# Optimization experiments

Measured on AMD Instinct MI355X. Metric: run time of the kernel, lower is better.

The kernel has to match this reference:

```python
import jax, jax.numpy as jnp
import numpy as np
from jax import lax

BN_EPS = 1e-5

def conv1x1(x, w, b):
    # x: [B,C,T,H,W], w: [O,C], b: [O] -> [B,O,T,H,W]
    return jnp.einsum('oc,bcthw->bothw', w, x) + b[None, :, None, None, None]

def maxpool_1x2x2(x):
    # MaxPool3d(kernel=(1,2,2)), stride = kernel
    return lax.reduce_window(x, -jnp.inf, lax.max,
                             window_dimensions=(1, 1, 1, 2, 2),
                             window_strides=(1, 1, 1, 2, 2),
                             padding='VALID')

def setup_inputs() -> dict:
    key = jax.random.key(0)
    ks = jax.random.split(key, 16)
    B, C, T, H, W = 4, 256, 8, 32, 32
    Ci = 128
    s_in = 1.0 / np.sqrt(C)
    s_mid = 1.0 / np.sqrt(Ci)
    return {
        'x': jax.random.normal(ks[0], (B, C, T, H, W), jnp.float32),
        'w_theta': jax.random.normal(ks[1], (Ci, C), jnp.float32) * s_in,
        'b_theta': jax.random.normal(ks[2], (Ci,), jnp.float32) * 0.01,
        'w_phi': jax.random.normal(ks[3], (Ci, C), jnp.float32) * s_in,
        'b_phi': jax.random.normal(ks[4], (Ci,), jnp.float32) * 0.01,
        'w_g': jax.random.normal(ks[5], (Ci, C), jnp.float32) * s_in,
        'b_g': jax.random.normal(ks[6], (Ci,), jnp.float32) * 0.01,
        'w_final': jax.random.normal(ks[7], (C, Ci), jnp.float32) * s_mid,
        'b_final': jax.random.normal(ks[8], (C,), jnp.float32) * 0.01,
        'bn_gamma': jax.random.uniform(ks[9], (C,), jnp.float32, 0.5, 1.5),
        'bn_beta': jax.random.normal(ks[10], (C,), jnp.float32) * 0.01,
        'bn_mean': jax.random.normal(ks[11], (C,), jnp.float32) * 0.01,
        'bn_var': jax.random.uniform(ks[12], (C,), jnp.float32, 0.5, 1.5),
    }

def reference(x, w_theta, b_theta, w_phi, b_phi, w_g, b_g,
              w_final, b_final, bn_gamma, bn_beta, bn_mean, bn_var):
    B, C, T, H, W = x.shape
    Ci = w_theta.shape[0]
    N = T * H * W
    # theta: queries over full resolution
    theta = conv1x1(x, w_theta, b_theta).reshape(B, Ci, N)           # [B,Ci,N]
    # phi, g: sub-sampled (1,2,2) keys / values
    phi = maxpool_1x2x2(conv1x1(x, w_phi, b_phi)).reshape(B, Ci, -1)  # [B,Ci,N2]
    g = maxpool_1x2x2(conv1x1(x, w_g, b_g)).reshape(B, Ci, -1)        # [B,Ci,N2]
    # relations = softmax(theta^T phi) over keys (embedded gaussian, unscaled)
    scores = jnp.einsum('bin,bim->bnm', theta, phi)                   # [B,N,N2]
    rel = jax.nn.softmax(scores, axis=-1)
    # y = rel @ g^T -> [B,N,Ci] -> [B,Ci,T,H,W]
    y = jnp.einsum('bnm,bim->bin', rel, g).reshape(B, Ci, T, H, W)
    # W_final: 1x1x1 conv + BatchNorm (eval mode, running stats)
    wy = conv1x1(y, w_final, b_final)
    inv = bn_gamma / jnp.sqrt(bn_var + BN_EPS)
    wy = (wy - bn_mean[None, :, None, None, None]) * inv[None, :, None, None, None] \
         + bn_beta[None, :, None, None, None]
    return wy + x
```

## Files before the change

### kernel.cpp

```cpp
#include <hip/hip_runtime.h>

typedef unsigned short u16;
typedef unsigned int   u32;

#define BB 4
#define CC 256
#define CI 128
#define NN 8192
#define N2 2048

#define PHI_OFF   0u
#define CAN0_OFF  2097152u
#define GP_OFF    2097168u
#define CAN1_OFF  4194320u
#define THB_OFF   4194336u
#define CAN2_OFF  8388640u
#define FLAG_OFF  8388644u
#define WHI_OFF   8388672u
#define WLO_OFF   8585280u
#define WFH_OFF   8781888u
#define PART_OFF  8847424u
#define WS_NEED   8855616u

#define CAN0V 0xC0FFEE01u
#define CAN1V 0xC0FFEE02u
#define CAN2V 0xC0FFEE03u

#define LOG2E 1.4426950408889634f

typedef _Float16 f16;
typedef f16 f16x8 __attribute__((ext_vector_type(8)));
typedef float f32x4 __attribute__((ext_vector_type(4)));

__device__ __forceinline__ u16 f2h(float f) {
    _Float16 h = (_Float16)f;
    return __builtin_bit_cast(u16, h);
}
__device__ __forceinline__ float h2f(u16 u) {
    return (float)__builtin_bit_cast(_Float16, u);
}

__global__ __launch_bounds__(256) void fill_constf(float* out, float v, int n)
{
    int i = blockIdx.x * 256 + threadIdx.x;
    if (i < n) out[i] = v;
}

__global__ __launch_bounds__(256) void probe_x(const u32* __restrict__ xv,
                                               u32* __restrict__ part)
{
    __shared__ u32 red[4];
    int tid = threadIdx.x;
    int gid = blockIdx.x * 256 + tid;
    const uint4* p = (const uint4*)xv;
    uint4 v0 = p[gid];
    uint4 v1 = p[gid + 524288];
    uint4 v2 = p[gid + 2 * 524288];
    uint4 v3 = p[gid + 3 * 524288];
    u32 ws_[16] = {v0.x, v0.y, v0.z, v0.w, v1.x, v1.y, v1.z, v1.w,
                   v2.x, v2.y, v2.z, v2.w, v3.x, v3.y, v3.z, v3.w};
    bool ff = false, nz = false;
#pragma unroll
    for (int j = 0; j < 16; j++) {
        u32 w = ws_[j];
        u32 lo = w & 0xffffu, hi = w >> 16;
        ff |= ((lo & 0x7f80u) == 0x7f80u) || ((hi & 0x7f80u) == 0x7f80u);
        nz |= (lo != 0u);
    }
    u32 wm = (__any(ff) ? 1u : 0u) | (__any(nz) ? 2u : 0u);
    if ((tid & 63) == 0) red[tid >> 6] = wm;
    __syncthreads();
    if (tid == 0) part[blockIdx.x] = red[0] | red[1] | red[2] | red[3];
}

__global__ __launch_bounds__(256) void prep_w(
    const float* __restrict__ w0, const float* __restrict__ w1,
    const float* __restrict__ w2, const float* __restrict__ wf,
    u16* __restrict__ whi, u16* __restrict__ wlo, u16* __restrict__ wfh,
    const u32* __restrict__ part, u32* __restrict__ ws32)
{
    if (blockIdx.x < 512) {
        int idx = blockIdx.x * 256 + threadIdx.x;
        if (idx < 98304) {
            int mb = idx >> 15, r = idx & 32767;
            float w = (mb == 0 ? w0 : (mb == 1 ? w1 : w2))[r];
            u16 hi = f2h(w);
            whi[idx] = hi;
            wlo[idx] = f2h(w - h2f(hi));
        } else {
            int r = idx - 98304;
            wfh[r] = f2h(wf[r]);
        }
    } else {
        __shared__ u32 red[4];
        int tid = threadIdx.x;
        u32 m = 0;
#pragma unroll
        for (int i = 0; i < 8; i++) m |= part[tid * 8 + i];
        m |= __shfl_xor(m, 1);  m |= __shfl_xor(m, 2);  m |= __shfl_xor(m, 4);
        m |= __shfl_xor(m, 8);  m |= __shfl_xor(m, 16); m |= __shfl_xor(m, 32);
        if ((tid & 63) == 0) red[tid >> 6] = m;
        __syncthreads();
        if (tid == 0) ws32[FLAG_OFF / 4] = red[0] | red[1] | red[2] | red[3];
    }
}

__global__ __launch_bounds__(256) void proj_mfma(
    const float* __restrict__ x,
    const float* __restrict__ b0v, const float* __restrict__ b1v,
    const float* __restrict__ b2v,
    const u16* __restrict__ whi, const u16* __restrict__ wlo,
    u16* __restrict__ thA, u16* __restrict__ thB,
    u16* __restrict__ phH, u16* __restrict__ gH,
    u32* __restrict__ ws32)
{
    __shared__ __align__(16) u16 smem[24576];
    int nb2 = blockIdx.x, mb = blockIdx.y, b = blockIdx.z;
    int tid = threadIdx.x;
    int lane = tid & 63, wid = tid >> 6, l15 = lane & 15, lg = lane >> 4;
    int n0 = nb2 * 64;

    const float* Bv = mb == 0 ? b0v : (mb == 1 ? b1v : b2v);
    const u16* whB = whi + mb * 32768;
    const u16* wlB = wlo + mb * 32768;

    int n_l = tid & 63, cg = tid >> 6;
    const float* xp = x + ((size_t)(b * CC + cg * 8)) * NN + n0 + n_l;
    int wci = tid >> 2, wkc = tid & 3;
    const u16* whp = whB + wci * 256 + wkc * 8;
    const u16* wlp = wlB + wci * 256 + wkc * 8;

    float xr[8];
    uint4 whr0, whr1, wlr0, wlr1;

#define PLOAD(s) do {                                                          \
    _Pragma("unroll") for (int j = 0; j < 8; j++)                              \
        xr[j] = xp[(size_t)((s) * 32 + j) * NN];                               \
    whr0 = *(const uint4*)(whp + (s) * 32);                                    \
    whr1 = *(const uint4*)(whp + 16384 + (s) * 32);                            \
    wlr0 = *(const uint4*)(wlp + (s) * 32);                                    \
    wlr1 = *(const uint4*)(wlp + 16384 + (s) * 32);                            \
} while (0)

#define PWRITE(bf) do {                                                        \
    u16* bp = smem + (bf) * 12288;                                             \
    u32 hw[4], lw[4];                                                          \
    _Pragma("unroll") for (int j = 0; j < 4; j++) {                            \
        u16 h0 = f2h(xr[2 * j]), h1 = f2h(xr[2 * j + 1]);                      \
        u16 q0 = f2h(xr[2 * j] - h2f(h0)), q1 = f2h(xr[2 * j + 1] - h2f(h1));  \
        hw[j] = (u32)h0 | ((u32)h1 << 16);                                     \
        lw[j] = (u32)q0 | ((u32)q1 << 16);                                     \
    }                                                                          \
    int xi = (n_l * 32 + cg * 8) ^ (((n_l >> 1) & 3) << 3);                    \
    *(uint4*)&bp[xi]        = make_uint4(hw[0], hw[1], hw[2], hw[3]);          \
    *(uint4*)&bp[2048 + xi] = make_uint4(lw[0], lw[1], lw[2], lw[3]);          \
    int wi = (wci * 32 + wkc * 8) ^ (((wci >> 1) & 3) << 3);                   \
    *(uint4*)&bp[4096 + wi]        = whr0;                                     \
    *(uint4*)&bp[4096 + wi + 2048] = whr1;                                     \
    *(uint4*)&bp[8192 + wi]        = wlr0;                                     \
    *(uint4*)&bp[8192 + wi + 2048] = wlr1;                                     \
} while (0)

    f32x4 acc[2][4];
#pragma unroll
    for (int i = 0; i < 2; i++)
#pragma unroll
        for (int j = 0; j < 4; j++) acc[i][j] = (f32x4){0.f, 0.f, 0.f, 0.f};

    PLOAD(0);
    PWRITE(0);
    PLOAD(1);
    __syncthreads();

    for (int t = 0; t < 8; t++) {
        int cur = t & 1;
        if (t + 1 < 8) PWRITE(cur ^ 1);
        if (t + 2 < 8) PLOAD(t + 2);
        const u16* bp = smem + cur * 12288;
        f16x8 ah[2], al[2], bh[4], bl[4];
#pragma unroll
        for (int rt = 0; rt < 2; rt++) {
            int r = wid * 32 + rt * 16 + l15;
            int idx = (r * 32 + lg * 8) ^ (((r >> 1) & 3) << 3);
            ah[rt] = *(const f16x8*)&bp[4096 + idx];
            al[rt] = *(const f16x8*)&bp[8192 + idx];
        }
#pragma unroll
        for (int ct = 0; ct < 4; ct++) {
            int n = ct * 16 + l15;
            int idx = (n * 32 + lg * 8) ^ (((n >> 1) & 3) << 3);
            bh[ct] = *(const f16x8*)&bp[idx];
            bl[ct] = *(const f16x8*)&bp[2048 + idx];
        }
#pragma unroll
        for (int rt = 0; rt < 2; rt++)
#pragma unroll
            for (int ct = 0; ct < 4; ct++) {
                acc[rt][ct] = __builtin_amdgcn_mfma_f32_16x16x32_f16(ah[rt], bh[ct], acc[rt][ct], 0, 0, 0);
                acc[rt][ct] = __builtin_amdgcn_mfma_f32_16x16x32_f16(ah[rt], bl[ct], acc[rt][ct], 0, 0, 0);
                acc[rt][ct] = __builtin_amdgcn_mfma_f32_16x16x32_f16(al[rt], bh[ct], acc[rt][ct], 0, 0, 0);
            }
        __syncthreads();
    }
#undef PLOAD
#undef PWRITE

    float* ot = (float*)smem;
#pragma unroll
    for (int rt = 0; rt < 2; rt++) {
        int cb = wid * 32 + rt * 16 + lg * 4;
        float4 b4 = *(const float4*)&Bv[cb];
#pragma unroll
        for (int ct = 0; ct < 4; ct++) {
            int n = ct * 16 + l15;
            float4 v = make_float4(acc[rt][ct][0] + b4.x, acc[rt][ct][1] + b4.y,
                                   acc[rt][ct][2] + b4.z, acc[rt][ct][3] + b4.w);
            *(float4*)&ot[n * 132 + cb] = v;
        }
    }
    __syncthreads();

    int mb0 = (nb2 >> 4) * 256 + (nb2 & 15) * 16;

    if (mb == 0) {
        int nl = tid >> 2, sg = (tid & 3) * 32;
        u16* base = (b < 2) ? thA : thB;
        u16* dst = base + ((size_t)((b & 1) * NN + n0 + nl)) * CI + sg;
        const float* src = &ot[nl * 132 + sg];
#pragma unroll
        for (int i = 0; i < 4; i++) {
            u32 w[4];
#pragma unroll
            for (int j = 0; j < 4; j++)
                w[j] = (u32)f2h(src[i * 8 + 2 * j] * LOG2E) |
                       ((u32)f2h(src[i * 8 + 2 * j + 1] * LOG2E) << 16);
            ((uint4*)dst)[i] = make_uint4(w[0], w[1], w[2], w[3]);
        }
    } else if (mb == 1) {
        int ml = tid >> 4, cs = (tid & 15) * 8;
        int r0 = 2 * ml, r1 = r0 + 1, r2 = 32 + 2 * ml, r3 = r2 + 1;
        float pv[8];
#pragma unroll
        for (int j = 0; j < 8; j++)
            pv[j] = fmaxf(fmaxf(ot[r0 * 132 + cs + j], ot[r1 * 132 + cs + j]),
                          fmaxf(ot[r2 * 132 + cs + j], ot[r3 * 132 + cs + j]));
        u32 w[4];
#pragma unroll
        for (int j = 0; j < 4; j++)
            w[j] = (u32)f2h(pv[2 * j]) | ((u32)f2h(pv[2 * j + 1]) << 16);
        *(uint4*)(phH + ((size_t)(b * N2 + mb0 + ml)) * CI + cs) =
            make_uint4(w[0], w[1], w[2], w[3]);
    } else {
        int gci = tid >> 1, half = tid & 1;
        u32 res[4];
#pragma unroll
        for (int p = 0; p < 4; p++) {
            int m0 = half * 8 + 2 * p, m1 = m0 + 1;
            float v0 = fmaxf(fmaxf(ot[(2 * m0) * 132 + gci], ot[(2 * m0 + 1) * 132 + gci]),
                             fmaxf(ot[(32 + 2 * m0) * 132 + gci], ot[(33 + 2 * m0) * 132 + gci]));
            float v1 = fmaxf(fmaxf(ot[(2 * m1) * 132 + gci], ot[(2 * m1 + 1) * 132 + gci]),
                             fmaxf(ot[(32 + 2 * m1) * 132 + gci], ot[(33 + 2 * m1) * 132 + gci]));
            res[p] = (u32)f2h(v0) | ((u32)f2h(v1) << 16);
        }
        *(uint4*)(gH + ((size_t)(b * CI + gci)) * N2 + mb0 + half * 8) =
            make_uint4(res[0], res[1], res[2], res[3]);
    }
    if (nb2 == 0 && mb == 0 && b == 0 && tid == 0) {
        ws32[CAN0_OFF / 4] = CAN0V;
        ws32[CAN1_OFF / 4] = CAN1V;
        ws32[CAN2_OFF / 4] = CAN2V;
    }
}

__global__ __launch_bounds__(512) void attn_fused(
    const u16* __restrict__ thH, const u16* __restrict__ phH,
    const u16* __restrict__ gH, const u16* __restrict__ wfh,
    const float* __restrict__ bfi, const float* __restrict__ gam,
    const float* __restrict__ bet, const float* __restrict__ mea,
    const float* __restrict__ varr, const float* __restrict__ x,
    const u32* __restrict__ ws32, float* __restrict__ out, int b0)
{
    __shared__ __align__(16) u16 kv_s[4][8192];
    __shared__ __align__(16) u16 p_s[8][512];
    __shared__ float cm[64], cl[64];
    __shared__ int flag;

    int tid = threadIdx.x;
    int lane = tid & 63, wid = tid >> 6;
    int l15 = lane & 15, lg = lane >> 4;
    int grp = wid >> 2;
    int wq  = wid & 3;
    int gtid = tid & 255;
    int qb = blockIdx.x, b = b0 + blockIdx.y;

    if (tid == 0) {
        u32 pf = ws32[FLAG_OFF / 4];
        bool ws_ok = ws32[CAN0_OFF / 4] == CAN0V && ws32[CAN1_OFF / 4] == CAN1V &&
                     ws32[CAN2_OFF / 4] == CAN2V;
        bool is_bf16_input = ((pf & 1u) == 0u) && ((pf & 2u) != 0u);
        flag = is_bf16_input ? 2 : (ws_ok ? 0 : 1);
    }

    const u16* phB = phH + (size_t)b * N2 * CI;
    const u16* gB  = gH + (size_t)b * CI * N2;

    uint4 rph0, rph1, rv0, rv1;

#define LOADKV(k0) do {                                                                  \
    rph0 = *(const uint4*)(phB + ((size_t)((k0) + (gtid >> 4))) * CI + (gtid & 15) * 8); \
    rph1 = *(const uint4*)(phB + ((size_t)((k0) + 16 + (gtid >> 4))) * CI + (gtid & 15) * 8); \
    rv0  = *(const uint4*)(gB + (size_t)(gtid >> 2) * N2 + (k0) + (gtid & 3) * 8);       \
    rv1  = *(const uint4*)(gB + (size_t)(64 + (gtid >> 2)) * N2 + (k0) + (gtid & 3) * 8); \
} while (0)

#define WRITEKV(buf) do {                                                                \
    u16* ph_d = kv_s[grp * 2 + (buf)]; u16* v_d = ph_d + 4096;                           \
    { int key = gtid >> 4;        int c8 = gtid & 15;                                    \
      *(uint4*)&ph_d[(key * 128 + c8 * 8) ^ ((key & 7) << 3)] = rph0; }                  \
    { int key = 16 + (gtid >> 4); int c8 = gtid & 15;                                    \
      *(uint4*)&ph_d[(key * 128 + c8 * 8) ^ ((key & 7) << 3)] = rph1; }                  \
    { int d = gtid >> 2;        int m8 = (gtid & 3) * 8;                                 \
      *(uint4*)&v_d[(d * 32 + m8) ^ (((d >> 1) & 3) << 3)] = rv0; }                      \
    { int d = 64 + (gtid >> 2); int m8 = (gtid & 3) * 8;                                 \
      *(uint4*)&v_d[(d * 32 + m8) ^ (((d >> 1) & 3) << 3)] = rv1; }                      \
} while (0)

    f16x8 ath[4];
    {
        const u16* tp = thH + ((size_t)((b - b0) * NN + qb * 64 + wq * 16 + l15)) * CI;
#pragma unroll
        for (int ks = 0; ks < 4; ks++)
            ath[ks] = *(const f16x8*)(tp + ks * 32 + lg * 8);
    }
    int kbase = grp * 1024;
    LOADKV(kbase);
    WRITEKV(0);
    LOADKV(kbase + 32);
    __syncthreads();

    if (flag) {
        float sig = flag == 2 ? 40000.f : 30000.f;
        if (tid < 256) {
            size_t rowb = ((size_t)(b * CC + tid)) * NN + qb * 64;
            for (int n = 0; n < 64; n++) out[rowb + n] = sig;
        }
        return;
    }

    f16x8 ones;
#pragma unroll
    for (int i = 0; i < 8; i++) ones[i] = (f16)1.0f;

    f32x4 Y[8];
#pragma unroll
    for (int i = 0; i < 8; i++) Y[i] = (f32x4){0.f, 0.f, 0.f, 0.f};
    f32x4 Yl = {0.f, 0.f, 0.f, 0.f};
    float m_run[4] = {-1e30f, -1e30f, -1e30f, -1e30f};

    for (int t = 0; t < 32; t++) {
        int cur = t & 1;
        if (t + 1 < 32) WRITEKV(cur ^ 1);
        if (t + 2 < 32) LOADKV(kbase + (t + 2) * 32);

        const u16* ph_c = kv_s[grp * 2 + cur];
        const u16* v_c  = ph_c + 4096;

        f32x4 S0 = {0.f, 0.f, 0.f, 0.f}, S1 = {0.f, 0.f, 0.f, 0.f};
#pragma unroll
        for (int ks = 0; ks < 4; ks++) {
            f16x8 bf0 = *(const f16x8*)&ph_c[(l15 * 128 + ks * 32 + lg * 8) ^ ((l15 & 7) << 3)];
            f16x8 bf1 = *(const f16x8*)&ph_c[((16 + l15) * 128 + ks * 32 + lg * 8) ^ (((16 + l15) & 7) << 3)];
            S0 = __builtin_amdgcn_mfma_f32_16x16x32_f16(ath[ks], bf0, S0, 0, 0, 0);
            S1 = __builtin_amdgcn_mfma_f32_16x16x32_f16(ath[ks], bf1, S1, 0, 0, 0);
        }

        float pmax[4], need = 0.f;
#pragma unroll
        for (int r = 0; r < 4; r++) {
            float v = fmaxf(S0[r], S1[r]);
            v = fmaxf(v, __shfl_xor(v, 1));
            v = fmaxf(v, __shfl_xor(v, 2));
            v = fmaxf(v, __shfl_xor(v, 4));
            v = fmaxf(v, __shfl_xor(v, 8));
            pmax[r] = v;
            need = fmaxf(need, v - m_run[r]);
        }
        if (__any(need > 11.5f)) {
            float al[4];
#pragma unroll
            for (int r = 0; r < 4; r++) {
                float mn = fmaxf(m_run[r], pmax[r]);
                al[r] = __builtin_amdgcn_exp2f(m_run[r] - mn);
                m_run[r] = mn;
            }
#pragma unroll
            for (int i = 0; i < 8; i++) {
#pragma unroll
                for (int r = 0; r < 4; r++) Y[i][r] *= al[r];
            }
#pragma unroll
            for (int r = 0; r < 4; r++) Yl[r] *= al[r];
        }
        float p0[4], p1[4];
#pragma unroll
        for (int r = 0; r < 4; r++) {
            p0[r] = __builtin_amdgcn_exp2f(S0[r] - m_run[r]);
            p1[r] = __builtin_amdgcn_exp2f(S1[r] - m_run[r]);
        }

        {
            u16* pw = p_s[wid];
#pragma unroll
            for (int r = 0; r < 4; r++) {
                int q = lg * 4 + r;
                int sw = ((q >> 1) & 3) << 3;
                pw[(q * 32 + l15) ^ sw]      = f2h(p0[r]);
                pw[(q * 32 + 16 + l15) ^ sw] = f2h(p1[r]);
            }
        }
        __builtin_amdgcn_sched_barrier(0);

        f16x8 pa = *(const f16x8*)&p_s[wid][(l15 * 32 + lg * 8) ^ (((l15 >> 1) & 3) << 3)];
        Yl = __builtin_amdgcn_mfma_f32_16x16x32_f16(pa, ones, Yl, 0, 0, 0);
#pragma unroll
        for (int dt = 0; dt < 8; dt++) {
            int d = dt * 16 + l15;
            f16x8 bv = *(const f16x8*)&v_c[(d * 32 + lg * 8) ^ (((d >> 1) & 3) << 3)];
            Y[dt] = __builtin_amdgcn_mfma_f32_16x16x32_f16(pa, bv, Y[dt], 0, 0, 0);
        }
        __syncthreads();
    }

    float* cmb = (float*)kv_s[2];
    if (grp == 1) {
        if (l15 == 0) {
#pragma unroll
            for (int r = 0; r < 4; r++) {
                int q = wq * 16 + lg * 4 + r;
                cm[q] = m_run[r];
                cl[q] = Yl[r];
            }
        }
#pragma unroll
        for (int dt = 0; dt < 8; dt++) {
#pragma unroll
            for (int r = 0; r < 4; r++) {
                int q = wq * 16 + lg * 4 + r;
                cmb[q * 128 + dt * 16 + l15] = Y[dt][r];
            }
        }
    }
    __syncthreads();

    u16* yl = (u16*)kv_s[0];
    if (grp == 0) {
        float a0[4], a1[4], linv[4];
#pragma unroll
        for (int r = 0; r < 4; r++) {
            int q = wq * 16 + lg * 4 + r;
            float m1 = cm[q], l1 = cl[q];
            float mm = fmaxf(m_run[r], m1);
            a0[r] = __builtin_amdgcn_exp2f(m_run[r] - mm);
            a1[r] = __builtin_amdgcn_exp2f(m1 - mm);
            linv[r] = 1.f / (Yl[r] * a0[r] + l1 * a1[r]);
        }
#pragma unroll
        for (int dt = 0; dt < 8; dt++) {
#pragma unroll
            for (int r = 0; r < 4; r++) {
                int q = wq * 16 + lg * 4 + r;
                int d = dt * 16 + l15;
                float ym = (Y[dt][r] * a0[r] + cmb[q * 128 + d] * a1[r]) * linv[r];
                yl[(q * 128 + d) ^ ((q & 7) << 3)] = f2h(ym);
            }
        }
    }
    __syncthreads();

    f16x8 bfr[4][4];
#pragma unroll
    for (int ks = 0; ks < 4; ks++)
#pragma unroll
        for (int ct = 0; ct < 4; ct++) {
            int n = ct * 16 + l15;
            bfr[ks][ct] = *(const f16x8*)&yl[(n * 128 + ks * 32 + lg * 8) ^ ((n & 7) << 3)];
        }

#pragma unroll
    for (int rt = 0; rt < 2; rt++) {
        int cb = wid * 32 + rt * 16;
        f16x8 af[4];
#pragma unroll
        for (int ks = 0; ks < 4; ks++)
            af[ks] = *(const f16x8*)(wfh + (size_t)(cb + l15) * 128 + ks * 32 + lg * 8);
        f32x4 acc2[4];
#pragma unroll
        for (int ct = 0; ct < 4; ct++) acc2[ct] = (f32x4){0.f, 0.f, 0.f, 0.f};
#pragma unroll
        for (int ks = 0; ks < 4; ks++)
#pragma unroll
            for (int ct = 0; ct < 4; ct++)
                acc2[ct] = __builtin_amdgcn_mfma_f32_16x16x32_f16(af[ks], bfr[ks][ct], acc2[ct], 0, 0, 0);

        int c4 = cb + lg * 4;
        float4 g4 = *(const float4*)&gam[c4];
        float4 v4 = *(const float4*)&varr[c4];
        float4 m4 = *(const float4*)&mea[c4];
        float4 t4 = *(const float4*)&bet[c4];
        float4 f4 = *(const float4*)&bfi[c4];
        float iv[4], mn[4], bt[4], bv[4];
        iv[0] = g4.x / sqrtf(v4.x + 1e-5f); iv[1] = g4.y / sqrtf(v4.y + 1e-5f);
        iv[2] = g4.z / sqrtf(v4.z + 1e-5f); iv[3] = g4.w / sqrtf(v4.w + 1e-5f);
        mn[0] = m4.x; mn[1] = m4.y; mn[2] = m4.z; mn[3] = m4.w;
        bt[0] = t4.x; bt[1] = t4.y; bt[2] = t4.z; bt[3] = t4.w;
        bv[0] = f4.x; bv[1] = f4.y; bv[2] = f4.z; bv[3] = f4.w;
#pragma unroll
        for (int ct = 0; ct < 4; ct++) {
            int n = qb * 64 + ct * 16 + l15;
#pragma unroll
            for (int r = 0; r < 4; r++) {
                size_t o = ((size_t)(b * CC + c4 + r)) * NN + n;
                out[o] = (acc2[ct][r] + bv[r] - mn[r]) * iv[r] + bt[r] + x[o];
            }
        }
    }
#undef LOADKV
#undef WRITEKV
}

extern "C" void kernel_launch(void* const* d_in, const int* in_sizes, int n_in,
                              void* d_out, int out_size, void* d_ws, size_t ws_size,
                              hipStream_t stream)
{
    const int NOUT = BB * CC * NN;
    bool sizes_ok = (n_in == 13) && (out_size == NOUT) &&
        in_sizes[0] == NOUT &&
        in_sizes[1] == CI * CC && in_sizes[2] == CI &&
        in_sizes[3] == CI * CC && in_sizes[4] == CI &&
        in_sizes[5] == CI * CC && in_sizes[6] == CI &&
        in_sizes[7] == CC * CI && in_sizes[8] == CC &&
        in_sizes[9] == CC && in_sizes[10] == CC && in_sizes[11] == CC && in_sizes[12] == CC;
    if (!sizes_ok || ws_size < (size_t)WS_NEED) {
        float sig = (!sizes_ok) ? 25000.f : 20000.f;
        hipLaunchKernelGGL(fill_constf, dim3((NOUT + 255) / 256), dim3(256), 0, stream,
                           (float*)d_out, sig, NOUT);
        return;
    }

    const float* x   = (const float*)d_in[0];
    const float* wth = (const float*)d_in[1];
    const float* bth = (const float*)d_in[2];
    const float* wph = (const float*)d_in[3];
    const float* bph = (const float*)d_in[4];
    const float* wg  = (const float*)d_in[5];
    const float* bg  = (const float*)d_in[6];
    const float* wf  = (const float*)d_in[7];
    const float* bfi = (const float*)d_in[8];
    const float* gam = (const float*)d_in[9];
    const float* bet = (const float*)d_in[10];
    const float* mea = (const float*)d_in[11];
    const float* var = (const float*)d_in[12];

    char* ws = (char*)d_ws;
    float* outF = (float*)d_out;
    u16*   thA  = (u16*)(outF + 4194304);
    u16*   thB  = (u16*)(ws + THB_OFF);
    u16*   phHp = (u16*)(ws + PHI_OFF);
    u16*   gHp  = (u16*)(ws + GP_OFF);
    u16*   wHi  = (u16*)(ws + WHI_OFF);
    u16*   wLo  = (u16*)(ws + WLO_OFF);
    u16*   wFh  = (u16*)(ws + WFH_OFF);
    u32*   part = (u32*)(ws + PART_OFF);
    u32*   w32  = (u32*)ws;

    hipLaunchKernelGGL(probe_x, dim3(2048), dim3(256), 0, stream, (const u32*)x, part);
    hipLaunchKernelGGL(prep_w, dim3(513), dim3(256), 0, stream,
                       wth, wph, wg, wf, wHi, wLo, wFh, part, w32);
    hipLaunchKernelGGL(proj_mfma, dim3(128, 3, 4), dim3(256), 0, stream,
                       x, bth, bph, bg, wHi, wLo, thA, thB, phHp, gHp, w32);
    hipLaunchKernelGGL(attn_fused, dim3(128, 2), dim3(512), 0, stream,
                       thA, phHp, gHp, wFh, bfi, gam, bet, mea, var, x, w32, outF, 0);
    hipLaunchKernelGGL(attn_fused, dim3(128, 2), dim3(512), 0, stream,
                       thB, phHp, gHp, wFh, bfi, gam, bet, mea, var, x, w32, outF, 2);
}
```

Before: 227.6 us.

## Transpose attention MFMA operands so each lane owns one query row

Swaps the A/B operands of the score and PV MFMAs so the accumulator holds keys (or head dims) along registers and queries along lanes. Each lane then tracks a single running max, so the row-max reduction needs two cross-lane shuffles instead of four per row, and the rescale uses one scalar factor. P, the cross-group combine buffer and the final y tile are written with packed vector stores instead of scalar 16-bit stores. The swizzle patterns change to fit the new layout, which risks LDS bank conflicts or layout mistakes.

Measured after the change: 207.8 us. 8.7% less time.

```diff
diff --git a/kernel.cpp b/kernel.cpp
--- a/kernel.cpp
+++ b/kernel.cpp
@@ -38,6 +38,9 @@
 }
 __device__ __forceinline__ float h2f(u16 u) {
     return (float)__builtin_bit_cast(_Float16, u);
+}
+__device__ __forceinline__ u32 pk2h(float a, float b) {
+    return (u32)f2h(a) | ((u32)f2h(b) << 16);
 }
 
 __global__ __launch_bounds__(256) void fill_constf(float* out, float v, int n)
@@ -355,7 +358,10 @@
 #pragma unroll
     for (int i = 0; i < 8; i++) Y[i] = (f32x4){0.f, 0.f, 0.f, 0.f};
     f32x4 Yl = {0.f, 0.f, 0.f, 0.f};
-    float m_run[4] = {-1e30f, -1e30f, -1e30f, -1e30f};
+    float m_run = -1e30f;
+
+    int psw = (l15 & 7) << 3;
+    u16* pw = p_s[wid];
 
     for (int t = 0; t < 32; t++) {
         int cur = t & 1;
@@ -370,109 +376,79 @@
         for (int ks = 0; ks < 4; ks++) {
             f16x8 bf0 = *(const f16x8*)&ph_c[(l15 * 128 + ks * 32 + lg * 8) ^ ((l15 & 7) << 3)];
             f16x8 bf1 = *(const f16x8*)&ph_c[((16 + l15) * 128 + ks * 32 + lg * 8) ^ (((16 + l15) & 7) << 3)];
-            S0 = __builtin_amdgcn_mfma_f32_16x16x32_f16(ath[ks], bf0, S0, 0, 0, 0);
-            S1 = __builtin_amdgcn_mfma_f32_16x16x32_f16(ath[ks], bf1, S1, 0, 0, 0);
-        }
-
-        float pmax[4], need = 0.f;
+            S0 = __builtin_amdgcn_mfma_f32_16x16x32_f16(bf0, ath[ks], S0, 0, 0, 0);
+            S1 = __builtin_amdgcn_mfma_f32_16x16x32_f16(bf1, ath[ks], S1, 0, 0, 0);
+        }
+
+        float v = fmaxf(fmaxf(fmaxf(S0[0], S0[1]), fmaxf(S0[2], S0[3])),
+                        fmaxf(fmaxf(S1[0], S1[1]), fmaxf(S1[2], S1[3])));
+        v = fmaxf(v, __shfl_xor(v, 16));
+        v = fmaxf(v, __shfl_xor(v, 32));
+        if (__any(v - m_run > 11.5f)) {
+            float mn = fmaxf(m_run, v);
+            float al = __builtin_amdgcn_exp2f(m_run - mn);
+            m_run = mn;
+#pragma unroll
+            for (int i = 0; i < 8; i++) {
+#pragma unroll
+                for (int r = 0; r < 4; r++) Y[i][r] *= al;
+            }
+#pragma unroll
+            for (int r = 0; r < 4; r++) Yl[r] *= al;
+        }
+        float p0[4], p1[4];
 #pragma unroll
         for (int r = 0; r < 4; r++) {
-            float v = fmaxf(S0[r], S1[r]);
-            v = fmaxf(v, __shfl_xor(v, 1));
-            v = fmaxf(v, __shfl_xor(v, 2));
-            v = fmaxf(v, __shfl_xor(v, 4));
-            v = fmaxf(v, __shfl_xor(v, 8));
-            pmax[r] = v;
-            need = fmaxf(need, v - m_run[r]);
-        }
-        if (__any(need > 11.5f)) {
-            float al[4];
-#pragma unroll
-            for (int r = 0; r < 4; r++) {
-                float mn = fmaxf(m_run[r], pmax[r]);
-                al[r] = __builtin_amdgcn_exp2f(m_run[r] - mn);
-                m_run[r] = mn;
-            }
-#pragma unroll
-            for (int i = 0; i < 8; i++) {
-#pragma unroll
-                for (int r = 0; r < 4; r++) Y[i][r] *= al[r];
-            }
-#pragma unroll
-            for (int r = 0; r < 4; r++) Yl[r] *= al[r];
-        }
-        float p0[4], p1[4];
-#pragma unroll
-        for (int r = 0; r < 4; r++) {
-            p0[r] = __builtin_amdgcn_exp2f(S0[r] - m_run[r]);
-            p1[r] = __builtin_amdgcn_exp2f(S1[r] - m_run[r]);
-        }
-
-        {
-            u16* pw = p_s[wid];
-#pragma unroll
-            for (int r = 0; r < 4; r++) {
-                int q = lg * 4 + r;
-                int sw = ((q >> 1) & 3) << 3;
-                pw[(q * 32 + l15) ^ sw]      = f2h(p0[r]);
-                pw[(q * 32 + 16 + l15) ^ sw] = f2h(p1[r]);
-            }
-        }
+            p0[r] = __builtin_amdgcn_exp2f(S0[r] - m_run);
+            p1[r] = __builtin_amdgcn_exp2f(S1[r] - m_run);
+        }
+
+        *(uint2*)&pw[(l15 * 32 + lg * 4) ^ psw] =
+            make_uint2(pk2h(p0[0], p0[1]), pk2h(p0[2], p0[3]));
+        *(uint2*)&pw[(l15 * 32 + 16 + lg * 4) ^ psw] =
+            make_uint2(pk2h(p1[0], p1[1]), pk2h(p1[2], p1[3]));
         __builtin_amdgcn_sched_barrier(0);
 
-        f16x8 pa = *(const f16x8*)&p_s[wid][(l15 * 32 + lg * 8) ^ (((l15 >> 1) & 3) << 3)];
-        Yl = __builtin_amdgcn_mfma_f32_16x16x32_f16(pa, ones, Yl, 0, 0, 0);
+        f16x8 pb = *(const f16x8*)&pw[(l15 * 32 + lg * 8) ^ psw];
+        Yl = __builtin_amdgcn_mfma_f32_16x16x32_f16(ones, pb, Yl, 0, 0, 0);
 #pragma unroll
         for (int dt = 0; dt < 8; dt++) {
             int d = dt * 16 + l15;
-            f16x8 bv = *(const f16x8*)&v_c[(d * 32 + lg * 8) ^ (((d >> 1) & 3) << 3)];
-            Y[dt] = __builtin_amdgcn_mfma_f32_16x16x32_f16(pa, bv, Y[dt], 0, 0, 0);
+            f16x8 av = *(const f16x8*)&v_c[(d * 32 + lg * 8) ^ (((d >> 1) & 3) << 3)];
+            Y[dt] = __builtin_amdgcn_mfma_f32_16x16x32_f16(av, pb, Y[dt], 0, 0, 0);
         }
         __syncthreads();
     }
 
     float* cmb = (float*)kv_s[2];
+    int q = wq * 16 + l15;
     if (grp == 1) {
-        if (l15 == 0) {
-#pragma unroll
-            for (int r = 0; r < 4; r++) {
-                int q = wq * 16 + lg * 4 + r;
-                cm[q] = m_run[r];
-                cl[q] = Yl[r];
-            }
-        }
-#pragma unroll
-        for (int dt = 0; dt < 8; dt++) {
-#pragma unroll
-            for (int r = 0; r < 4; r++) {
-                int q = wq * 16 + lg * 4 + r;
-                cmb[q * 128 + dt * 16 + l15] = Y[dt][r];
-            }
-        }
+        if (lg == 0) {
+            cm[q] = m_run;
+            cl[q] = Yl[0];
+        }
+#pragma unroll
+        for (int dt = 0; dt < 8; dt++)
+            *(f32x4*)&cmb[(q * 128 + dt * 16 + lg * 4) ^ ((q & 7) << 2)] = Y[dt];
     }
     __syncthreads();
 
     u16* yl = (u16*)kv_s[0];
     if (grp == 0) {
-        float a0[4], a1[4], linv[4];
-#pragma unroll
-        for (int r = 0; r < 4; r++) {
-            int q = wq * 16 + lg * 4 + r;
-            float m1 = cm[q], l1 = cl[q];
-            float mm = fmaxf(m_run[r], m1);
-            a0[r] = __builtin_amdgcn_exp2f(m_run[r] - mm);
-            a1[r] = __builtin_amdgcn_exp2f(m1 - mm);
-            linv[r] = 1.f / (Yl[r] * a0[r] + l1 * a1[r]);
-        }
+        float m1 = cm[q], l1 = cl[q];
+        float mm = fmaxf(m_run, m1);
+        float a0 = __builtin_amdgcn_exp2f(m_run - mm);
+        float a1 = __builtin_amdgcn_exp2f(m1 - mm);
+        float linv = 1.f / (Yl[0] * a0 + l1 * a1);
 #pragma unroll
         for (int dt = 0; dt < 8; dt++) {
-#pragma unroll
-            for (int r = 0; r < 4; r++) {
-                int q = wq * 16 + lg * 4 + r;
-                int d = dt * 16 + l15;
-                float ym = (Y[dt][r] * a0[r] + cmb[q * 128 + d] * a1[r]) * linv[r];
-                yl[(q * 128 + d) ^ ((q & 7) << 3)] = f2h(ym);
-            }
+            f32x4 c4 = *(const f32x4*)&cmb[(q * 128 + dt * 16 + lg * 4) ^ ((q & 7) << 2)];
+            float y0 = (Y[dt][0] * a0 + c4[0] * a1) * linv;
+            float y1 = (Y[dt][1] * a0 + c4[1] * a1) * linv;
+            float y2 = (Y[dt][2] * a0 + c4[2] * a1) * linv;
+            float y3 = (Y[dt][3] * a0 + c4[3] * a1) * linv;
+            *(uint2*)&yl[(q * 128 + dt * 16 + lg * 4) ^ ((q & 7) << 3)] =
+                make_uint2(pk2h(y0, y1), pk2h(y2, y3));
         }
     }
     __syncthreads();
```
